# Performance work log

Measured on AMD Instinct MI355X. Metric: run time of the kernel, lower is better.

## Reference

```python
import jax, jax.numpy as jnp
import numpy as np

B, S, D = 8, 1024, 768
H, DK, DV = 12, 64, 64
NEG = -1e12


def setup_inputs() -> dict:
    key = jax.random.key(0)
    ks = jax.random.split(key, 8)
    s = 0.02
    return {
        "x": jax.random.normal(ks[0], (B, S, D), jnp.float32),
        "Wq": jax.random.normal(ks[1], (D, H * DK), jnp.float32) * s,
        "bq": jnp.zeros((H * DK,), jnp.float32),
        "Wk": jax.random.normal(ks[2], (D, H * DK), jnp.float32) * s,
        "bk": jnp.zeros((H * DK,), jnp.float32),
        "Wv": jax.random.normal(ks[3], (D, H * DV), jnp.float32) * s,
        "bv": jnp.zeros((H * DV,), jnp.float32),
        "Wo": jax.random.normal(ks[4], (H * DV, D), jnp.float32) * s,
        "bo": jnp.zeros((D,), jnp.float32),
        "position_bias": jax.random.normal(ks[5], (S, S, DK), jnp.float32) * s,
        "q_mask": jnp.ones((B, S), jnp.float32),
        "v_mask": jnp.ones((B, S), jnp.float32),
    }


def reference(x, Wq, bq, Wk, bk, Wv, bv, Wo, bo, position_bias, q_mask, v_mask):
    b, s, _ = x.shape
    qw = (x @ Wq + bq).reshape(b, s, H, DK)  # [b,s,h,dk]
    kw = (x @ Wk + bk).reshape(b, s, H, DK)
    vw = (x @ Wv + bv).reshape(b, s, H, DV)
    # scores with fused typical_relative position bias
    a = jnp.einsum("bjhd,bkhd->bhjk", qw, kw)
    a = a + jnp.einsum("bjhd,jkd->bhjk", qw, position_bias)
    a = a / jnp.sqrt(jnp.float32(DK))
    # mask keys (v_mask): additive -1e12 on padded positions
    a = a + (1.0 - v_mask)[:, None, None, :] * NEG
    A = jax.nn.softmax(a, axis=-1)
    o = jnp.einsum("bhjk,bkhd->bjhd", A, vw)
    o = o + jnp.einsum("bhjk,jkd->bjhd", A, position_bias)
    o = o.reshape(b, s, H * DV)
    o = o @ Wo + bo
    # zero out padded query positions (q_mask, multiplicative)
    o = o * q_mask[:, :, None]
    return o
```

## Files before the change

### kernel.cpp

```cpp
#include <hip/hip_runtime.h>

#define B_  8
#define S_  1024
#define D_  768
#define H_  12
#define DK_ 64
#define BH_ 96

typedef _Float16 f16;
typedef _Float16 f16x8 __attribute__((ext_vector_type(8)));
typedef _Float16 f16x4 __attribute__((ext_vector_type(4)));
typedef float    f32x4 __attribute__((ext_vector_type(4)));

#define MFMA16(a, b, c) __builtin_amdgcn_mfma_f32_16x16x32_f16((a), (b), (c), 0, 0, 0)

__device__ __forceinline__ int swz(int row) { return ((row ^ (row >> 3)) & 7) << 4; }

__device__ __forceinline__ f16x8 lds_read8(const f16* base, int row, int rowbytes, int colbyte) {
    const char* p = (const char*)base + row * rowbytes + (colbyte ^ swz(row));
    return *(const f16x8*)p;
}
__device__ __forceinline__ void lds_write8(f16* base, int row, int rowbytes, int colbyte, f16x8 v) {
    char* p = (char*)base + row * rowbytes + (colbyte ^ swz(row));
    *(f16x8*)p = v;
}
__device__ __forceinline__ void lds_write4(f16* base, int row, int rowbytes, int colbyte, f16x4 v) {
    char* p = (char*)base + row * rowbytes + (colbyte ^ swz(row));
    *(f16x4*)p = v;
}
__device__ __forceinline__ void lds_write1(f16* base, int row, int rowbytes, int colbyte, f16 v) {
    char* p = (char*)base + row * rowbytes + (colbyte ^ swz(row));
    *(f16*)p = v;
}
__device__ __forceinline__ f16 lds_read1(const f16* base, int row, int rowbytes, int colbyte) {
    const char* p = (const char*)base + row * rowbytes + (colbyte ^ swz(row));
    return *(const f16*)p;
}

__global__ __launch_bounds__(256) void cvt_x(const float* __restrict__ in,
                                             f16* __restrict__ out, int n4)
{
    const int i = blockIdx.x * 256 + threadIdx.x;
    if (i < n4) {
        const float4 v = ((const float4*)in)[i];
        f16x4 h; h[0] = (f16)v.x; h[1] = (f16)v.y; h[2] = (f16)v.z; h[3] = (f16)v.w;
        ((f16x4*)out)[i] = h;
    }
}

__global__ __launch_bounds__(256) void wT_cvt(
    const float* __restrict__ Wq, const float* __restrict__ Wk,
    const float* __restrict__ Wv, const float* __restrict__ Wo,
    f16* __restrict__ Tq, f16* __restrict__ Tk,
    f16* __restrict__ Tv, f16* __restrict__ To)
{
    const float* W; f16* T;
    if      (blockIdx.z == 0) { W = Wq; T = Tq; }
    else if (blockIdx.z == 1) { W = Wk; T = Tk; }
    else if (blockIdx.z == 2) { W = Wv; T = Tv; }
    else                      { W = Wo; T = To; }

    const int r0 = blockIdx.x * 32;
    const int c0 = blockIdx.y * 32;
    const int t = threadIdx.x, tx = t & 31, ty = t >> 5;

    __shared__ float tile[32][33];
    #pragma unroll
    for (int i = 0; i < 4; ++i)
        tile[ty + 8 * i][tx] = W[(size_t)(r0 + ty + 8 * i) * D_ + c0 + tx];
    __syncthreads();
    #pragma unroll
    for (int i = 0; i < 4; ++i)
        T[(size_t)(c0 + ty + 8 * i) * D_ + r0 + tx] = (f16)tile[tx][ty + 8 * i];
}

__global__ __launch_bounds__(256) void qkv_mfma(
    const f16* __restrict__ x16,
    const f16* __restrict__ Tq, const f16* __restrict__ Tk, const f16* __restrict__ Tv,
    const float* __restrict__ bq, const float* __restrict__ bk, const float* __restrict__ bv,
    f16* __restrict__ qo, f16* __restrict__ ko, f16* __restrict__ vo)
{
    const f16* WT; const float* bias; f16* out; float scale;
    if      (blockIdx.z == 0) { WT = Tq; bias = bq; out = qo; scale = 0.125f; }
    else if (blockIdx.z == 1) { WT = Tk; bias = bk; out = ko; scale = 1.0f; }
    else                      { WT = Tv; bias = bv; out = vo; scale = 1.0f; }

    const int row0 = blockIdx.x * 128;
    const int col0 = blockIdx.y * 128;
    const int t = threadIdx.x, l = t & 63, w = t >> 6;
    const int wr = w >> 1, wc = w & 1;

    __shared__ __attribute__((aligned(16))) f16 As[128 * 64];
    __shared__ __attribute__((aligned(16))) f16 Bs[128 * 64];

    f32x4 acc[4][4] = {};

    for (int kt = 0; kt < D_; kt += 64) {
        __syncthreads();
        #pragma unroll
        for (int ii = 0; ii < 4; ++ii) {
            const int idx = t + ii * 256;
            const int r = idx >> 3, c8 = idx & 7;
            f16x8 v = *(const f16x8*)(x16 + (size_t)(row0 + r) * D_ + kt + c8 * 8);
            lds_write8(As, r, 128, c8 * 16, v);
        }
        #pragma unroll
        for (int ii = 0; ii < 4; ++ii) {
            const int idx = t + ii * 256;
            const int r = idx >> 3, c8 = idx & 7;
            f16x8 v = *(const f16x8*)(WT + (size_t)(col0 + r) * D_ + kt + c8 * 8);
            lds_write8(Bs, r, 128, c8 * 16, v);
        }
        __syncthreads();
        #pragma unroll
        for (int ks = 0; ks < 2; ++ks) {
            f16x8 af[4], bf[4];
            #pragma unroll
            for (int mi = 0; mi < 4; ++mi)
                af[mi] = lds_read8(As, wr * 64 + mi * 16 + (l & 15), 128, ks * 64 + (l >> 4) * 16);
            #pragma unroll
            for (int ni = 0; ni < 4; ++ni)
                bf[ni] = lds_read8(Bs, wc * 64 + ni * 16 + (l & 15), 128, ks * 64 + (l >> 4) * 16);
            #pragma unroll
            for (int mi = 0; mi < 4; ++mi)
                #pragma unroll
                for (int ni = 0; ni < 4; ++ni)
                    acc[mi][ni] = MFMA16(af[mi], bf[ni], acc[mi][ni]);
        }
    }

    #pragma unroll
    for (int mi = 0; mi < 4; ++mi)
        #pragma unroll
        for (int q = 0; q < 4; ++q) {
            const int row = row0 + wr * 64 + mi * 16 + (l >> 4) * 4 + q;
            const int b = row >> 10, s = row & 1023;
            #pragma unroll
            for (int ni = 0; ni < 4; ++ni) {
                const int col = col0 + wc * 64 + ni * 16 + (l & 15);
                const int h = col >> 6, dk = col & 63;
                out[(((size_t)(b * H_ + h)) * S_ + s) * DK_ + dk] = (f16)((acc[mi][ni][q] + bias[col]) * scale);
            }
        }
}

__global__ __launch_bounds__(256) void vT_cvt(const f16* __restrict__ V, f16* __restrict__ Vt)
{
    const int bh = blockIdx.x;
    const int s0 = blockIdx.y * 64;
    const int t = threadIdx.x;
    __shared__ __attribute__((aligned(16))) f16 tile[64 * 64];
    #pragma unroll
    for (int ii = 0; ii < 2; ++ii) {
        const int u = t + ii * 256;
        const int r = u >> 3, c8 = u & 7;
        f16x8 v = *(const f16x8*)(V + ((size_t)bh * S_ + s0 + r) * DK_ + c8 * 8);
        lds_write8(tile, r, 128, c8 * 16, v);
    }
    __syncthreads();
    #pragma unroll
    for (int ii = 0; ii < 2; ++ii) {
        const int u = t + ii * 256;
        const int d = u >> 3, sc = u & 7;
        f16x8 o;
        #pragma unroll
        for (int e = 0; e < 8; ++e) o[e] = lds_read1(tile, sc * 8 + e, 128, d * 2);
        *(f16x8*)(Vt + ((size_t)bh * DK_ + d) * S_ + s0 + sc * 8) = o;
    }
}

__global__ __launch_bounds__(256) void s2_gemm(
    const f16* __restrict__ Qb, const float* __restrict__ pb,
    f16* __restrict__ S2, f16* __restrict__ pbT)
{
    const int j  = blockIdx.x;
    const int n0 = blockIdx.y * 256;
    const int t = threadIdx.x, l = t & 63, w = t >> 6;

    __shared__ __attribute__((aligned(16))) f16 Ps[256 * 64];

    for (int idx = t; idx < 256 * 16; idx += 256) {
        const int r = idx >> 4, c4 = idx & 15;
        const float4 v = *(const float4*)(pb + ((size_t)j * S_ + n0 + r) * DK_ + c4 * 4);
        f16x4 h; h[0] = (f16)v.x; h[1] = (f16)v.y; h[2] = (f16)v.z; h[3] = (f16)v.w;
        lds_write4(Ps, r, 128, c4 * 8, h);
    }

    f16x8 qf[6][2];
    #pragma unroll
    for (int mi = 0; mi < 6; ++mi)
        #pragma unroll
        for (int ks = 0; ks < 2; ++ks)
            qf[mi][ks] = *(const f16x8*)(Qb + ((size_t)(mi * 16 + (l & 15)) * S_ + j) * DK_ + ks * 32 + (l >> 4) * 8);

    __syncthreads();

    f32x4 acc[6][4] = {};
    #pragma unroll
    for (int s = 0; s < 4; ++s) {
        const int nrow = w * 64 + s * 16 + (l & 15);
        const f16x8 b0 = lds_read8(Ps, nrow, 128, (l >> 4) * 16);
        const f16x8 b1 = lds_read8(Ps, nrow, 128, 64 + (l >> 4) * 16);
        #pragma unroll
        for (int mi = 0; mi < 6; ++mi) {
            acc[mi][s] = MFMA16(qf[mi][0], b0, acc[mi][s]);
            acc[mi][s] = MFMA16(qf[mi][1], b1, acc[mi][s]);
        }
    }

    #pragma unroll
    for (int mi = 0; mi < 6; ++mi)
        #pragma unroll
        for (int q = 0; q < 4; ++q) {
            const int bh = mi * 16 + (l >> 4) * 4 + q;
            const size_t base = (size_t)bh * (S_ * S_) + (size_t)j * S_;
            #pragma unroll
            for (int s = 0; s < 4; ++s) {
                const int k = n0 + w * 64 + s * 16 + (l & 15);
                S2[base + k] = (f16)acc[mi][s][q];
            }
        }

    #pragma unroll
    for (int ii = 0; ii < 8; ++ii) {
        const int u = t + ii * 256;
        const int d = u >> 5, kc = u & 31;
        f16x8 o;
        #pragma unroll
        for (int e = 0; e < 8; ++e) o[e] = lds_read1(Ps, kc * 8 + e, 128, d * 2);
        *(f16x8*)(pbT + ((size_t)j * DK_ + d) * S_ + n0 + kc * 8) = o;
    }
}

__global__ __launch_bounds__(256) void attn_sm(
    const f16* __restrict__ Qb, const f16* __restrict__ Kb,
    const float* __restrict__ vmask, f16* __restrict__ S2A)
{
    const int j0 = blockIdx.x * 16;
    const int bh = blockIdx.y, b = bh / H_;
    const int t = threadIdx.x, l = t & 63, w = t >> 6;

    __shared__ __attribute__((aligned(16))) f16 SA[16 * 1024];
    __shared__ f16 mflag[1024];
    __shared__ float redm[4][16], reds[4][16];

    for (int idx = t; idx < 16 * 128; idx += 256) {
        const int r = idx >> 7, c8 = idx & 127;
        f16x8 v = *(const f16x8*)(S2A + (size_t)bh * (S_ * S_) + (size_t)(j0 + r) * S_ + c8 * 8);
        lds_write8(SA, r, 2048, c8 * 16, v);
    }
    for (int k = t; k < 1024; k += 256)
        mflag[k] = (f16)(1.0f - vmask[(size_t)b * S_ + k]);

    const f16x8 aq0 = *(const f16x8*)(Qb + ((size_t)bh * S_ + j0 + (l & 15)) * DK_ + (l >> 4) * 8);
    const f16x8 aq1 = *(const f16x8*)(Qb + ((size_t)bh * S_ + j0 + (l & 15)) * DK_ + 32 + (l >> 4) * 8);
    __syncthreads();

    f32x4 acc[16] = {};
    #pragma unroll
    for (int f = 0; f < 16; ++f) {
        const int k = (f >> 1) * 128 + w * 32 + (f & 1) * 16 + (l & 15);
        const f16* kp = Kb + ((size_t)bh * S_ + k) * DK_ + (l >> 4) * 8;
        const f16x8 b0 = *(const f16x8*)kp;
        const f16x8 b1 = *(const f16x8*)(kp + 32);
        acc[f] = MFMA16(aq0, b0, acc[f]);
        acc[f] = MFMA16(aq1, b1, acc[f]);
    }

    float mrow[4] = {-3e38f, -3e38f, -3e38f, -3e38f};
    #pragma unroll
    for (int f = 0; f < 16; ++f) {
        const int k = (f >> 1) * 128 + w * 32 + (f & 1) * 16 + (l & 15);
        const float vm = (float)mflag[k] * -30000.0f;
        #pragma unroll
        for (int q = 0; q < 4; ++q) {
            const int r = (l >> 4) * 4 + q;
            const float s2v = (float)lds_read1(SA, r, 2048, k * 2);
            const float val = acc[f][q] + s2v + vm;
            acc[f][q] = val;
            mrow[q] = fmaxf(mrow[q], val);
        }
    }
    #pragma unroll
    for (int q = 0; q < 4; ++q) {
        float m = mrow[q];
        #pragma unroll
        for (int off = 1; off < 16; off <<= 1) m = fmaxf(m, __shfl_xor(m, off));
        mrow[q] = m;
    }
    if ((l & 15) == 0) {
        #pragma unroll
        for (int q = 0; q < 4; ++q) redm[w][(l >> 4) * 4 + q] = mrow[q];
    }
    __syncthreads();
    #pragma unroll
    for (int q = 0; q < 4; ++q) {
        const int r = (l >> 4) * 4 + q;
        mrow[q] = fmaxf(fmaxf(redm[0][r], redm[1][r]), fmaxf(redm[2][r], redm[3][r]));
    }

    float lsum[4] = {0.f, 0.f, 0.f, 0.f};
    #pragma unroll
    for (int f = 0; f < 16; ++f)
        #pragma unroll
        for (int q = 0; q < 4; ++q) {
            const float e = __expf(acc[f][q] - mrow[q]);
            acc[f][q] = e;
            lsum[q] += e;
        }
    #pragma unroll
    for (int q = 0; q < 4; ++q) {
        float s = lsum[q];
        #pragma unroll
        for (int off = 1; off < 16; off <<= 1) s += __shfl_xor(s, off);
        lsum[q] = s;
    }
    if ((l & 15) == 0) {
        #pragma unroll
        for (int q = 0; q < 4; ++q) reds[w][(l >> 4) * 4 + q] = lsum[q];
    }
    __syncthreads();
    #pragma unroll
    for (int q = 0; q < 4; ++q) {
        const int r = (l >> 4) * 4 + q;
        lsum[q] = 1.0f / (reds[0][r] + reds[1][r] + reds[2][r] + reds[3][r]);
    }

    #pragma unroll
    for (int q = 0; q < 4; ++q) {
        const int r = (l >> 4) * 4 + q;
        #pragma unroll
        for (int f = 0; f < 16; ++f) {
            const int k = (f >> 1) * 128 + w * 32 + (f & 1) * 16 + (l & 15);
            lds_write1(SA, r, 2048, k * 2, (f16)(acc[f][q] * lsum[q]));
        }
    }
    __syncthreads();

    for (int idx = t; idx < 16 * 128; idx += 256) {
        const int r = idx >> 7, c8 = idx & 127;
        const f16x8 v = lds_read8(SA, r, 2048, c8 * 16);
        *(f16x8*)(S2A + (size_t)bh * (S_ * S_) + (size_t)(j0 + r) * S_ + c8 * 8) = v;
    }
}

__global__ __launch_bounds__(256) void av_gemm(
    const f16* __restrict__ A, const f16* __restrict__ Vt,
    float* __restrict__ omid)
{
    const int j0 = blockIdx.x * 64;
    const int bh = blockIdx.y, b = bh / H_, h = bh % H_;
    const int t = threadIdx.x, l = t & 63, w = t >> 6;

    const f16* abase = A + (size_t)bh * (S_ * S_) + (size_t)(j0 + w * 16 + (l & 15)) * S_ + (l >> 4) * 8;
    const f16* vbase = Vt + (size_t)bh * DK_ * S_ + (size_t)(l & 15) * S_ + (l >> 4) * 8;

    f32x4 acc[4] = {};
    #pragma unroll 4
    for (int ks = 0; ks < 32; ++ks) {
        const f16x8 af = *(const f16x8*)(abase + ks * 32);
        #pragma unroll
        for (int ni = 0; ni < 4; ++ni) {
            const f16x8 vf = *(const f16x8*)(vbase + (size_t)(ni * 16) * S_ + ks * 32);
            acc[ni] = MFMA16(af, vf, acc[ni]);
        }
    }

    #pragma unroll
    for (int ni = 0; ni < 4; ++ni)
        #pragma unroll
        for (int q = 0; q < 4; ++q) {
            const int j = j0 + w * 16 + (l >> 4) * 4 + q;
            const int d = ni * 16 + (l & 15);
            omid[((size_t)b * S_ + j) * D_ + h * DK_ + d] = acc[ni][q];
        }
}

__global__ __launch_bounds__(256) void apb_gemm(
    const f16* __restrict__ A, const f16* __restrict__ pbT,
    const float* __restrict__ omid, f16* __restrict__ omid16)
{
    const int j = blockIdx.x;
    const int t = threadIdx.x, l = t & 63, w = t >> 6;

    const f16* abase = A + (size_t)(l & 15) * (S_ * S_) + (size_t)j * S_ + (l >> 4) * 8;
    const f16* bbase = pbT + ((size_t)j * DK_ + w * 16 + (l & 15)) * S_ + (l >> 4) * 8;

    f32x4 acc[6] = {};
    #pragma unroll 4
    for (int ks = 0; ks < 32; ++ks) {
        const f16x8 bf = *(const f16x8*)(bbase + ks * 32);
        #pragma unroll
        for (int mi = 0; mi < 6; ++mi) {
            const f16x8 af = *(const f16x8*)(abase + (size_t)(mi * 16) * (S_ * S_) + ks * 32);
            acc[mi] = MFMA16(af, bf, acc[mi]);
        }
    }

    #pragma unroll
    for (int mi = 0; mi < 6; ++mi)
        #pragma unroll
        for (int q = 0; q < 4; ++q) {
            const int bh = mi * 16 + (l >> 4) * 4 + q;
            const int b = bh / H_, h = bh % H_;
            const int d = w * 16 + (l & 15);
            const size_t o = ((size_t)b * S_ + j) * D_ + h * DK_ + d;
            omid16[o] = (f16)(omid[o] + acc[mi][q]);
        }
}

__global__ __launch_bounds__(256) void out_mfma(
    const f16* __restrict__ a16, const f16* __restrict__ WT,
    const float* __restrict__ bias, const float* __restrict__ qm,
    float* __restrict__ out)
{
    const int row0 = blockIdx.x * 128;
    const int col0 = blockIdx.y * 128;
    const int t = threadIdx.x, l = t & 63, w = t >> 6;
    const int wr = w >> 1, wc = w & 1;

    __shared__ __attribute__((aligned(16))) f16 As[128 * 64];
    __shared__ __attribute__((aligned(16))) f16 Bs[128 * 64];

    f32x4 acc[4][4] = {};

    for (int kt = 0; kt < D_; kt += 64) {
        __syncthreads();
        #pragma unroll
        for (int ii = 0; ii < 4; ++ii) {
            const int idx = t + ii * 256;
            const int r = idx >> 3, c8 = idx & 7;
            f16x8 v = *(const f16x8*)(a16 + (size_t)(row0 + r) * D_ + kt + c8 * 8);
            lds_write8(As, r, 128, c8 * 16, v);
        }
        #pragma unroll
        for (int ii = 0; ii < 4; ++ii) {
            const int idx = t + ii * 256;
            const int r = idx >> 3, c8 = idx & 7;
            f16x8 v = *(const f16x8*)(WT + (size_t)(col0 + r) * D_ + kt + c8 * 8);
            lds_write8(Bs, r, 128, c8 * 16, v);
        }
        __syncthreads();
        #pragma unroll
        for (int ks = 0; ks < 2; ++ks) {
            f16x8 af[4], bf[4];
            #pragma unroll
            for (int mi = 0; mi < 4; ++mi)
                af[mi] = lds_read8(As, wr * 64 + mi * 16 + (l & 15), 128, ks * 64 + (l >> 4) * 16);
            #pragma unroll
            for (int ni = 0; ni < 4; ++ni)
                bf[ni] = lds_read8(Bs, wc * 64 + ni * 16 + (l & 15), 128, ks * 64 + (l >> 4) * 16);
            #pragma unroll
            for (int mi = 0; mi < 4; ++mi)
                #pragma unroll
                for (int ni = 0; ni < 4; ++ni)
                    acc[mi][ni] = MFMA16(af[mi], bf[ni], acc[mi][ni]);
        }
    }

    #pragma unroll
    for (int mi = 0; mi < 4; ++mi)
        #pragma unroll
        for (int q = 0; q < 4; ++q) {
            const int row = row0 + wr * 64 + mi * 16 + (l >> 4) * 4 + q;
            const float qmv = qm[row];
            #pragma unroll
            for (int ni = 0; ni < 4; ++ni) {
                const int col = col0 + wc * 64 + ni * 16 + (l & 15);
                out[(size_t)row * D_ + col] = (acc[mi][ni][q] + bias[col]) * qmv;
            }
        }
}

extern "C" void kernel_launch(void* const* d_in, const int* in_sizes, int n_in,
                              void* d_out, int out_size, void* d_ws, size_t ws_size,
                              hipStream_t stream) {
    const float* x  = (const float*)d_in[0];
    const float* Wq = (const float*)d_in[1];
    const float* bq = (const float*)d_in[2];
    const float* Wk = (const float*)d_in[3];
    const float* bk = (const float*)d_in[4];
    const float* Wv = (const float*)d_in[5];
    const float* bv = (const float*)d_in[6];
    const float* Wo = (const float*)d_in[7];
    const float* bo = (const float*)d_in[8];
    const float* pb = (const float*)d_in[9];
    const float* qm = (const float*)d_in[10];
    const float* vm = (const float*)d_in[11];
    float* out = (float*)d_out;

    const size_t NQ = (size_t)BH_ * S_ * DK_;
    const size_t NW = (size_t)D_ * D_;
    f16* qb  = (f16*)d_ws;
    f16* kb  = qb + NQ;
    f16* vb  = kb + NQ;
    f16* vt  = vb + NQ;
    f16* s2  = vt + NQ;
    f16* pbT = s2 + (size_t)BH_ * S_ * S_;
    f16* x16 = pbT + (size_t)S_ * DK_ * S_;
    f16* tq  = x16 + (size_t)B_ * S_ * D_;
    f16* tk  = tq + NW;
    f16* tv  = tk + NW;
    f16* to  = tv + NW;
    f16* omid16 = to + NW;
    float* omid = (float*)(omid16 + (size_t)B_ * S_ * D_);

    cvt_x<<<dim3((B_ * S_ * D_ / 4 + 255) / 256), 256, 0, stream>>>(x, x16, B_ * S_ * D_ / 4);
    wT_cvt<<<dim3(24, 24, 4), 256, 0, stream>>>(Wq, Wk, Wv, Wo, tq, tk, tv, to);

    qkv_mfma<<<dim3(64, 6, 3), 256, 0, stream>>>(x16, tq, tk, tv, bq, bk, bv, qb, kb, vb);
    vT_cvt<<<dim3(96, 16), 256, 0, stream>>>(vb, vt);

    s2_gemm <<<dim3(1024, 4), 256, 0, stream>>>(qb, pb, s2, pbT);
    attn_sm <<<dim3(64, 96),  256, 0, stream>>>(qb, kb, vm, s2);
    av_gemm <<<dim3(16, 96),  256, 0, stream>>>(s2, vt, omid);
    apb_gemm<<<dim3(1024),    256, 0, stream>>>(s2, pbT, omid, omid16);

    out_mfma<<<dim3(64, 6), 256, 0, stream>>>(omid16, to, bo, qm, out);
}
```

Baseline: 694.0 us.

## Store score matrix in fragment-native tiled layout to drop LDS staging in softmax

The shared S2/A score buffer changes from row-major [bh][j][k] to a tiled layout that matches the MFMA accumulator fragment order used by attn_sm. attn_sm can then read the position-bias scores and write the probabilities directly per lane from global memory, removing the 32KB LDS staging buffer, its swizzled copies and a barrier. The producer (score/pbias kernel) and both consumers (av_gemm, apb_gemm) are updated to compute addresses in the new layout. The cost is that some global accesses become scattered 2-byte accesses or less contiguous f16x8 loads. Lower LDS use may also raise occupancy.

```diff
diff --git a/kernel.cpp b/kernel.cpp
--- a/kernel.cpp
+++ b/kernel.cpp
@@ -37,6 +37,7 @@
     return *(const f16*)p;
 }
 
+
 __global__ __launch_bounds__(256) void cvt_x(const float* __restrict__ in,
                                              f16* __restrict__ out, int n4)
 {
@@ -208,16 +209,19 @@
         }
     }
 
+    const int jt = j >> 4, qj = j & 3, rh = (j >> 2) & 3;
     #pragma unroll
     for (int mi = 0; mi < 6; ++mi)
         #pragma unroll
         for (int q = 0; q < 4; ++q) {
             const int bh = mi * 16 + (l >> 4) * 4 + q;
-            const size_t base = (size_t)bh * (S_ * S_) + (size_t)j * S_;
+            const size_t bhbase = ((size_t)bh << 20) + ((size_t)jt << 14);
             #pragma unroll
             for (int s = 0; s < 4; ++s) {
                 const int k = n0 + w * 64 + s * 16 + (l & 15);
-                S2[base + k] = (f16)acc[mi][s][q];
+                const int kw = (k >> 5) & 3;
+                const int ff = 2 * (k >> 7) + ((k >> 4) & 1);
+                S2[bhbase + (size_t)(((kw * 16 + ff) * 4 + qj) * 64 + rh * 16 + (k & 15))] = (f16)acc[mi][s][q];
             }
         }
 
@@ -240,15 +244,9 @@
     const int bh = blockIdx.y, b = bh / H_;
     const int t = threadIdx.x, l = t & 63, w = t >> 6;
 
-    __shared__ __attribute__((aligned(16))) f16 SA[16 * 1024];
     __shared__ f16 mflag[1024];
     __shared__ float redm[4][16], reds[4][16];
 
-    for (int idx = t; idx < 16 * 128; idx += 256) {
-        const int r = idx >> 7, c8 = idx & 127;
-        f16x8 v = *(const f16x8*)(S2A + (size_t)bh * (S_ * S_) + (size_t)(j0 + r) * S_ + c8 * 8);
-        lds_write8(SA, r, 2048, c8 * 16, v);
-    }
     for (int k = t; k < 1024; k += 256)
         mflag[k] = (f16)(1.0f - vmask[(size_t)b * S_ + k]);
 
@@ -267,6 +265,7 @@
         acc[f] = MFMA16(aq1, b1, acc[f]);
     }
 
+    const size_t fbase = ((size_t)bh << 20) + ((size_t)(j0 >> 4) << 14) + l;
     float mrow[4] = {-3e38f, -3e38f, -3e38f, -3e38f};
     #pragma unroll
     for (int f = 0; f < 16; ++f) {
@@ -274,8 +273,7 @@
         const float vm = (float)mflag[k] * -30000.0f;
         #pragma unroll
         for (int q = 0; q < 4; ++q) {
-            const int r = (l >> 4) * 4 + q;
-            const float s2v = (float)lds_read1(SA, r, 2048, k * 2);
+            const float s2v = (float)S2A[fbase + (size_t)(((w * 16 + f) * 4 + q) * 64)];
             const float val = acc[f][q] + s2v + vm;
             acc[f][q] = val;
             mrow[q] = fmaxf(mrow[q], val);
@@ -327,21 +325,10 @@
     }
 
     #pragma unroll
-    for (int q = 0; q < 4; ++q) {
-        const int r = (l >> 4) * 4 + q;
-        #pragma unroll
-        for (int f = 0; f < 16; ++f) {
-            const int k = (f >> 1) * 128 + w * 32 + (f & 1) * 16 + (l & 15);
-            lds_write1(SA, r, 2048, k * 2, (f16)(acc[f][q] * lsum[q]));
-        }
-    }
-    __syncthreads();
-
-    for (int idx = t; idx < 16 * 128; idx += 256) {
-        const int r = idx >> 7, c8 = idx & 127;
-        const f16x8 v = lds_read8(SA, r, 2048, c8 * 16);
-        *(f16x8*)(S2A + (size_t)bh * (S_ * S_) + (size_t)(j0 + r) * S_ + c8 * 8) = v;
-    }
+    for (int f = 0; f < 16; ++f)
+        #pragma unroll
+        for (int q = 0; q < 4; ++q)
+            S2A[fbase + (size_t)(((w * 16 + f) * 4 + q) * 64)] = (f16)(acc[f][q] * lsum[q]);
 }
 
 __global__ __launch_bounds__(256) void av_gemm(
@@ -352,13 +339,20 @@
     const int bh = blockIdx.y, b = bh / H_, h = bh % H_;
     const int t = threadIdx.x, l = t & 63, w = t >> 6;
 
-    const f16* abase = A + (size_t)bh * (S_ * S_) + (size_t)(j0 + w * 16 + (l & 15)) * S_ + (l >> 4) * 8;
+    const int jt   = (j0 >> 4) + w;
+    const int qj   = l & 3;
+    const int rh   = (l & 15) >> 2;
+    const int k0lo = ((l >> 4) & 1) * 8;
+    const int fhi  = l >> 5;
+
+    const f16* abase = A + ((size_t)bh << 20) + ((size_t)jt << 14) + rh * 16 + k0lo;
     const f16* vbase = Vt + (size_t)bh * DK_ * S_ + (size_t)(l & 15) * S_ + (l >> 4) * 8;
 
     f32x4 acc[4] = {};
     #pragma unroll 4
     for (int ks = 0; ks < 32; ++ks) {
-        const f16x8 af = *(const f16x8*)(abase + ks * 32);
+        const int ff = 2 * (ks >> 2) + fhi;
+        const f16x8 af = *(const f16x8*)(abase + (size_t)((((ks & 3) * 16 + ff) * 4 + qj) * 64));
         #pragma unroll
         for (int ni = 0; ni < 4; ++ni) {
             const f16x8 vf = *(const f16x8*)(vbase + (size_t)(ni * 16) * S_ + ks * 32);
@@ -383,16 +377,23 @@
     const int j = blockIdx.x;
     const int t = threadIdx.x, l = t & 63, w = t >> 6;
 
-    const f16* abase = A + (size_t)(l & 15) * (S_ * S_) + (size_t)j * S_ + (l >> 4) * 8;
+    const int qj   = j & 3;
+    const int rh   = (j >> 2) & 3;
+    const int k0lo = ((l >> 4) & 1) * 8;
+    const int fhi  = l >> 5;
+
+    const f16* abase = A + ((size_t)(j >> 4) << 14) + rh * 16 + k0lo;
     const f16* bbase = pbT + ((size_t)j * DK_ + w * 16 + (l & 15)) * S_ + (l >> 4) * 8;
 
     f32x4 acc[6] = {};
     #pragma unroll 4
     for (int ks = 0; ks < 32; ++ks) {
+        const int ff = 2 * (ks >> 2) + fhi;
+        const size_t koff = (size_t)((((ks & 3) * 16 + ff) * 4 + qj) * 64);
         const f16x8 bf = *(const f16x8*)(bbase + ks * 32);
         #pragma unroll
         for (int mi = 0; mi < 6; ++mi) {
-            const f16x8 af = *(const f16x8*)(abase + (size_t)(mi * 16) * (S_ * S_) + ks * 32);
+            const f16x8 af = *(const f16x8*)(abase + ((size_t)(mi * 16 + (l & 15)) << 20) + koff);
             acc[mi] = MFMA16(af, bf, acc[mi]);
         }
     }
```

New measurement: 858.5 us. 1.24x slower.
